# Kernel tuning notes

Measured on AMD Instinct MI355X. Metric: run time of the kernel, lower is better.

The kernel has to match this reference:

```python
import jax, jax.numpy as jnp
import numpy as np

N_NODES = 100000
N_EDGES = 1600000
N_GRAPHS = 512
EPS = 1e-12


def _glorot(key, shape):
    lim = float(np.sqrt(6.0 / (shape[0] + shape[1])))
    return jax.random.uniform(key, shape, jnp.float32, -lim, lim)


def setup_inputs() -> dict:
    key = jax.random.key(0)
    ks = jax.random.split(key, 16)
    x = jax.random.normal(ks[0], (N_NODES, 5), jnp.float32)
    edge_index = jax.random.randint(ks[1], (2, N_EDGES), 0, N_NODES)
    batch = jnp.sort(jax.random.randint(ks[2], (N_NODES,), 0, N_GRAPHS))
    return {
        "x": x,
        "edge_index": edge_index,
        "batch": batch,
        "num_graphs": N_GRAPHS,
        # pre: Linear(5, 32)
        "pre_w": _glorot(ks[3], (5, 32)), "pre_b": jnp.zeros((32,), jnp.float32),
        # conv1: SAGEConv(32, 64): lin_l (agg, bias), lin_r (root, no bias)
        "c1_wl": _glorot(ks[4], (32, 64)), "c1_bl": jnp.zeros((64,), jnp.float32),
        "c1_wr": _glorot(ks[5], (32, 64)),
        # conv2: SAGEConv(64, 64)
        "c2_wl": _glorot(ks[6], (64, 64)), "c2_bl": jnp.zeros((64,), jnp.float32),
        "c2_wr": _glorot(ks[7], (64, 64)),
        # post / out linears
        "p1_w": _glorot(ks[8], (64, 64)), "p1_b": jnp.zeros((64,), jnp.float32),
        "p2_w": _glorot(ks[9], (64, 16)), "p2_b": jnp.zeros((16,), jnp.float32),
        "o_w": _glorot(ks[10], (16, 1)), "o_b": jnp.zeros((1,), jnp.float32),
    }


def _sage_conv(x, src, dst, w_l, b_l, w_r, n_nodes):
    # mean-aggregate neighbor messages src -> dst
    msg = x[src]                                              # [E, d]
    agg = jax.ops.segment_sum(msg, dst, num_segments=n_nodes)  # [N, d]
    cnt = jax.ops.segment_sum(jnp.ones((src.shape[0], 1), x.dtype), dst,
                              num_segments=n_nodes)            # [N, 1]
    agg = jnp.where(cnt > 0, agg / jnp.maximum(cnt, 1.0), 0.0)
    out = agg @ w_l + b_l + x @ w_r
    # normalize=True -> L2 normalize per node
    nrm = jnp.linalg.norm(out, axis=-1, keepdims=True)
    return out / jnp.maximum(nrm, EPS)


def reference(x, edge_index, batch, num_graphs,
              pre_w, pre_b, c1_wl, c1_bl, c1_wr, c2_wl, c2_bl, c2_wr,
              p1_w, p1_b, p2_w, p2_b, o_w, o_b):
    n_nodes = x.shape[0]
    src, dst = edge_index[0], edge_index[1]
    h = jax.nn.relu(x @ pre_w + pre_b)
    h = jax.nn.relu(_sage_conv(h, src, dst, c1_wl, c1_bl, c1_wr, n_nodes))
    h = jax.nn.relu(_sage_conv(h, src, dst, c2_wl, c2_bl, c2_wr, n_nodes))
    # global mean pool over batch index
    s = jax.ops.segment_sum(h, batch, num_segments=num_graphs)          # [G, d]
    c = jax.ops.segment_sum(jnp.ones((n_nodes, 1), h.dtype), batch,
                            num_segments=num_graphs)                    # [G, 1]
    g = s / jnp.maximum(c, 1.0)
    g = jax.nn.relu(g @ p1_w + p1_b)
    g = jax.nn.relu(g @ p2_w + p2_b)
    out = g @ o_w + o_b
    return out.squeeze(-1)
```

## Files before the change

### kernel.cpp

```cpp
#include <hip/hip_runtime.h>

#define EPSN 1e-12f
#define TILE 2048
#define BSH 8
#define BNODES 256
#define SBMAX 512
#define BCAP 4608
#define CSRCAP 512

using frag_ab = __attribute__((ext_vector_type(8))) short;
using frag_cd = __attribute__((ext_vector_type(4))) float;
using f32x2   = __attribute__((ext_vector_type(2))) float;

template <bool B> struct BoolC { static constexpr bool value = B; };

__device__ inline unsigned short f2bf(float x) {
    union { float f; unsigned u; } v; v.f = x;
    unsigned r = v.u + 0x7fffu + ((v.u >> 16) & 1u);
    return (unsigned short)(r >> 16);
}
__device__ inline unsigned short pk2fp8(float a, float b) {
    return (unsigned short)(__builtin_amdgcn_cvt_pk_fp8_f32(a, b, 0, false) & 0xffff);
}
__device__ inline unsigned char to_fp8(float a) {
    return (unsigned char)(__builtin_amdgcn_cvt_pk_fp8_f32(a, a, 0, false) & 0xff);
}
__device__ inline void up8add(unsigned u, float* a) {
    f32x2 lo = __builtin_amdgcn_cvt_pk_f32_fp8(u, false);
    f32x2 hi = __builtin_amdgcn_cvt_pk_f32_fp8(u, true);
    a[0] += lo.x; a[1] += lo.y; a[2] += hi.x; a[3] += hi.y;
}

__global__ __launch_bounds__(256) void prep_all(
    const float* __restrict__ x, const float* __restrict__ pw,
    const float* __restrict__ pb, unsigned char* __restrict__ h0, int n,
    const float* __restrict__ w1l, const float* __restrict__ w1r,
    unsigned short* __restrict__ wpk1,
    const float* __restrict__ w2l, const float* __restrict__ w2r,
    unsigned short* __restrict__ wpk2,
    float* __restrict__ sg, int gtot,
    int* __restrict__ bcnt, int nsb) {
    int idx = blockIdx.x * 256 + threadIdx.x;
    int npre = n * 16;
    if (idx < npre) {
        int node = idx >> 4, j2 = idx & 15;
        int j = j2 * 2;
        float v0 = pb[j], v1 = pb[j + 1];
#pragma unroll
        for (int k = 0; k < 5; ++k) {
            float xv = x[node * 5 + k];
            v0 += xv * pw[k * 32 + j];
            v1 += xv * pw[k * 32 + j + 1];
        }
        ((unsigned short*)h0)[node * 16 + j2] =
            pk2fp8(fmaxf(v0, 0.f), fmaxf(v1, 0.f));
        return;
    }
    int o = idx - npre;
    if (o < 64 * 64) {
        int j = o / 64, k = o % 64;
        float v = (k < 32) ? w1l[k * 64 + j] : w1r[(k - 32) * 64 + j];
        wpk1[o] = f2bf(v);
        return;
    }
    o -= 64 * 64;
    if (o < 64 * 128) {
        int j = o / 128, k = o % 128;
        float v = (k < 64) ? w2l[k * 64 + j] : w2r[(k - 64) * 64 + j];
        wpk2[o] = f2bf(v);
        return;
    }
    o -= 64 * 128;
    if (o < gtot) { sg[o] = 0.f; return; }
    o -= gtot;
    if (o < nsb) bcnt[o] = 0;
}

__global__ __launch_bounds__(256) void scat1_k(const int* __restrict__ src,
                                               const int* __restrict__ dst,
                                               int* __restrict__ bcnt,
                                               int* __restrict__ staged, int e,
                                               int nsb) {
    __shared__ int lh[SBMAX];
    __shared__ int cur[SBMAX];
    int tid = threadIdx.x;
    for (int i = tid; i < nsb; i += 256) lh[i] = 0;
    __syncthreads();
    int base = blockIdx.x * TILE;
    int lim = min(base + TILE, e);
    for (int i = base + tid; i < lim; i += 256) atomicAdd(&lh[dst[i] >> BSH], 1);
    __syncthreads();
    for (int i = tid; i < nsb; i += 256) {
        int c = lh[i];
        int b = 0;
        if (c) b = atomicAdd(&bcnt[i], c);
        cur[i] = i * BCAP + b;
    }
    __syncthreads();
    for (int i = base + tid; i < lim; i += 256) {
        int d = dst[i];
        int p = atomicAdd(&cur[d >> BSH], 1);
        staged[p] = (src[i] << BSH) | (d & (BNODES - 1));
    }
}

__global__ __launch_bounds__(256) void scat2_k(const int* __restrict__ btot,
                                               const int* __restrict__ staged,
                                               int* __restrict__ csr,
                                               int* __restrict__ rofs,
                                               int* __restrict__ deg,
                                               int n, int nsb) {
    __shared__ int h[BNODES];
    __shared__ int cur[BNODES];
    __shared__ int wsum[8];
    int b = blockIdx.x;
    int tid = threadIdx.x;
    int lane = tid & 63, w = tid >> 6;
    int nlo = b << BSH;
    int nn = n - nlo; if (nn > BNODES) nn = BNODES;
    int lo = b * BCAP, hi = lo + btot[b];
    h[tid] = 0;
    __syncthreads();
    for (int i = lo + tid; i < hi; i += 256) atomicAdd(&h[staged[i] & (BNODES - 1)], 1);
    __syncthreads();
    int x = h[tid];
    int inc = x;
#pragma unroll
    for (int o = 1; o < 64; o <<= 1) {
        int t = __shfl_up(inc, o);
        if (lane >= o) inc += t;
    }
    if (lane == 63) wsum[w] = inc;
    __syncthreads();
    if (tid == 0) {
        int s = 0;
#pragma unroll
        for (int k = 0; k < 4; ++k) { int t = wsum[k]; wsum[k] = s; s += t; }
    }
    __syncthreads();
    int excl = inc - x + wsum[w];
    cur[tid] = excl;
    if (tid < nn) {
        rofs[nlo + tid] = lo + excl;
        deg[nlo + tid] = x;
    }
    __syncthreads();
    for (int i = lo + tid; i < hi; i += 256) {
        int v = staged[i];
        int p = atomicAdd(&cur[v & (BNODES - 1)], 1);
        csr[lo + p] = v >> BSH;
    }
}

template <int KE, bool POOL>
__global__ __launch_bounds__(256) void conv_mfma(
    const int* __restrict__ rofs, const int* __restrict__ deg,
    const int* __restrict__ csr,
    const unsigned char* __restrict__ hin, const unsigned short* __restrict__ wpk,
    const float* __restrict__ bl, const int* __restrict__ batch,
    float* __restrict__ sg, unsigned char* __restrict__ hout, int n) {
    constexpr int KT = 2 * KE;
    constexpr int ST = KT + 8;
    constexpr int KS = KT / 32;
    constexpr int LPE = KE / 4;
    constexpr int EPW = 64 / LPE;
    constexpr int RB = 16 / EPW;
    constexpr bool G4 = (LPE == 16);
    __shared__ unsigned short __attribute__((aligned(16))) Ab[16 * ST];
    __shared__ float __attribute__((aligned(16))) Nb[4][16];
    __shared__ int ro[16];
    __shared__ int dg[16];
    __shared__ int sb[16];
    __shared__ int csrL[CSRCAP];

    int tid = threadIdx.x;
    int w = tid >> 6;
    int lane = tid & 63;
    int quad = lane >> 4;
    int l16 = lane & 15;
    int base = blockIdx.x * 16;
    int ncol = w * 16 + l16;

    if (tid < 16) {
        int nd = base + tid;
        bool v = nd < n;
        ro[tid] = v ? rofs[nd] : 0;
        dg[tid] = v ? deg[nd] : 0;
        if (POOL) sb[tid] = v ? batch[nd] : -1;
    }

    frag_ab bfrag[KS];
#pragma unroll
    for (int s = 0; s < KS; ++s)
        bfrag[s] = *(const frag_ab*)&wpk[(((ncol * KS) + s) * 4 + quad) * 8];
    float bias = bl[ncol];
    __syncthreads();

    int ro0 = ro[0];
    int lastv = min(15, n - 1 - base);
    int span = ro[lastv] + dg[lastv] - ro0;
    int spanL = min(span, CSRCAP);
    for (int i = tid; i < spanL; i += 256) csrL[i] = csr[ro0 + i];

    int grp = lane / LPE;
    int p = lane % LPE;
    int beg[4], cnt[4];
#pragma unroll
    for (int i = 0; i < 4; ++i) {
        int li = w * 4 + i;
        beg[i] = ro[li] - ro0;
        cnt[i] = dg[li];
    }

    int sn = G4 ? grp : (grp & 3);
    bool doSelf = G4 || (grp >= 4);
    bool doAgg = G4 || (grp < 4);
    int snode = base + w * 4 + sn;
    unsigned selfv = 0u;
    if (doSelf && snode < n)
        selfv = *(const unsigned*)&hin[(size_t)snode * KE + p * 4];
    __syncthreads();

    float A[4][4] = {{0.f, 0.f, 0.f, 0.f}, {0.f, 0.f, 0.f, 0.f},
                     {0.f, 0.f, 0.f, 0.f}, {0.f, 0.f, 0.f, 0.f}};

    auto run_sweeps = [&](auto uselc) {
        constexpr bool USEL = decltype(uselc)::value;
        for (int s = 0;; ++s) {
            int e0 = s * 16;
            unsigned u[4][RB];
            bool act[4];
#pragma unroll
            for (int i = 0; i < 4; ++i) {
                act[i] = e0 < cnt[i];
                if (act[i]) {
#pragma unroll
                    for (int r = 0; r < RB; ++r) {
                        int ee = e0 + r * EPW + grp;
                        int cl = (ee < cnt[i]) ? ee : (cnt[i] - 1);
                        int off = beg[i] + cl;
                        int idx;
                        if (USEL || off < CSRCAP) idx = csrL[off];
                        else idx = csr[ro0 + off];
                        u[i][r] = *(const unsigned*)&hin[(size_t)idx * KE + p * 4];
                    }
                }
            }
#pragma unroll
            for (int i = 0; i < 4; ++i) {
                if (act[i]) {
#pragma unroll
                    for (int r = 0; r < RB; ++r)
                        if (e0 + r * EPW + grp < cnt[i]) up8add(u[i][r], A[i]);
                }
            }
            bool more = false;
#pragma unroll
            for (int i = 0; i < 4; ++i) more |= (e0 + 16) < cnt[i];
            if (!more) break;
        }
    };
    if (span <= CSRCAP) run_sweeps(BoolC<true>{});
    else run_sweeps(BoolC<false>{});

#pragma unroll
    for (int i = 0; i < 4; ++i) {
#pragma unroll
        for (int o = LPE; o < 64; o <<= 1) {
#pragma unroll
            for (int q = 0; q < 4; ++q) A[i][q] += __shfl_xor(A[i][q], o);
        }
    }

    float av0 = A[0][0], av1 = A[0][1], av2 = A[0][2], av3 = A[0][3];
    int cs = cnt[0];
#pragma unroll
    for (int i = 1; i < 4; ++i) {
        bool m = (sn == i);
        av0 = m ? A[i][0] : av0; av1 = m ? A[i][1] : av1;
        av2 = m ? A[i][2] : av2; av3 = m ? A[i][3] : av3;
        cs = m ? cnt[i] : cs;
    }
    {
        int li = w * 4 + sn;
        int node = base + li;
        if (node < n) {
            if (doAgg) {
                float inv = (cs > 0) ? 1.0f / (float)cs : 0.0f;
                uint2 o2;
                o2.x = (unsigned)f2bf(av0 * inv) | ((unsigned)f2bf(av1 * inv) << 16);
                o2.y = (unsigned)f2bf(av2 * inv) | ((unsigned)f2bf(av3 * inv) << 16);
                *(uint2*)&Ab[li * ST + p * 4] = o2;
            }
            if (doSelf) {
                f32x2 lo = __builtin_amdgcn_cvt_pk_f32_fp8(selfv, false);
                f32x2 hi = __builtin_amdgcn_cvt_pk_f32_fp8(selfv, true);
                uint2 o2;
                o2.x = (unsigned)f2bf(lo.x) | ((unsigned)f2bf(lo.y) << 16);
                o2.y = (unsigned)f2bf(hi.x) | ((unsigned)f2bf(hi.y) << 16);
                *(uint2*)&Ab[li * ST + KE + p * 4] = o2;
            }
        }
    }
    __syncthreads();

    frag_cd acc = (frag_cd){0.f, 0.f, 0.f, 0.f};
#pragma unroll
    for (int s = 0; s < KS; ++s) {
        frag_ab af = *(frag_ab*)&Ab[l16 * ST + s * 32 + quad * 8];
        acc = __builtin_amdgcn_mfma_f32_16x16x32_bf16(af, bfrag[s], acc, 0, 0, 0);
    }

    float vv[4], q[4];
#pragma unroll
    for (int i = 0; i < 4; ++i) {
        float v = acc[i] + bias;
        vv[i] = v;
        q[i] = v * v;
    }
#pragma unroll
    for (int o = 1; o < 16; o <<= 1) {
#pragma unroll
        for (int i = 0; i < 4; ++i) q[i] += __shfl_xor(q[i], o);
    }
    if (l16 == 0)
        *(float4*)&Nb[w][quad * 4] = make_float4(q[0], q[1], q[2], q[3]);
    __syncthreads();

    float s0 = 0.f, s1 = 0.f, s2 = 0.f, s3 = 0.f;
#pragma unroll
    for (int ww = 0; ww < 4; ++ww) {
        float4 xq = *(const float4*)&Nb[ww][quad * 4];
        s0 += xq.x; s1 += xq.y; s2 += xq.z; s3 += xq.w;
    }
    float ss[4] = {s0, s1, s2, s3};
    float pv[4];
#pragma unroll
    for (int i = 0; i < 4; ++i) {
        float nv = fmaxf(sqrtf(ss[i]), EPSN);
        pv[i] = fmaxf(vv[i] / nv, 0.f);
    }

    if (!POOL) {
#pragma unroll
        for (int i = 0; i < 4; ++i) {
            int node = base + quad * 4 + i;
            if (node < n)
                hout[(size_t)node * 64 + ncol] = to_fp8(pv[i]);
        }
    } else {
        int g0 = sb[0];
        int g1 = sb[min(15, n - 1 - base)];
        for (int g = g0; g <= g1; ++g) {
            float s = 0.f;
#pragma unroll
            for (int i = 0; i < 4; ++i)
                if (sb[quad * 4 + i] == g) s += pv[i];
            s += __shfl_xor(s, 16);
            s += __shfl_xor(s, 32);
            if (quad == 0) atomicAdd(&sg[(size_t)g * 64 + ncol], s);
        }
    }
}

__global__ __launch_bounds__(64) void mlp_k(
    const float* __restrict__ sg, const int* __restrict__ batch, int n,
    const float* __restrict__ p1w, const float* __restrict__ p1b,
    const float* __restrict__ p2w, const float* __restrict__ p2b,
    const float* __restrict__ ow, const float* __restrict__ ob,
    float* __restrict__ out) {
    __shared__ float gmean[64];
    __shared__ float a1[64];
    __shared__ float a2[16];
    int g = blockIdx.x;
    int j = threadIdx.x;
    int lo = 0, hi = n;
    while (lo < hi) { int m = (lo + hi) >> 1; if (batch[m] < g) lo = m + 1; else hi = m; }
    int start = lo;
    hi = n;
    while (lo < hi) { int m = (lo + hi) >> 1; if (batch[m] < g + 1) lo = m + 1; else hi = m; }
    float c = (float)(lo - start);
    gmean[j] = sg[(size_t)g * 64 + j] / fmaxf(c, 1.0f);
    __syncthreads();
    float v = p1b[j];
#pragma unroll 8
    for (int k = 0; k < 64; ++k) v = fmaf(gmean[k], p1w[k * 64 + j], v);
    a1[j] = fmaxf(v, 0.f);
    __syncthreads();
    if (j < 16) {
        float v2 = p2b[j];
#pragma unroll 8
        for (int k = 0; k < 64; ++k) v2 = fmaf(a1[k], p2w[k * 16 + j], v2);
        a2[j] = fmaxf(v2, 0.f);
    }
    __syncthreads();
    if (j == 0) {
        float v3 = ob[0];
#pragma unroll
        for (int k = 0; k < 16; ++k) v3 = fmaf(a2[k], ow[k], v3);
        out[g] = v3;
    }
}

extern "C" void kernel_launch(void* const* d_in, const int* in_sizes, int n_in,
                              void* d_out, int out_size, void* d_ws, size_t ws_size,
                              hipStream_t stream) {
    const float* x     = (const float*)d_in[0];
    const int*   ei    = (const int*)d_in[1];
    const int*   batch = (const int*)d_in[2];
    const float* pre_w = (const float*)d_in[4];
    const float* pre_b = (const float*)d_in[5];
    const float* c1_wl = (const float*)d_in[6];
    const float* c1_bl = (const float*)d_in[7];
    const float* c1_wr = (const float*)d_in[8];
    const float* c2_wl = (const float*)d_in[9];
    const float* c2_bl = (const float*)d_in[10];
    const float* c2_wr = (const float*)d_in[11];
    const float* p1w   = (const float*)d_in[12];
    const float* p1b   = (const float*)d_in[13];
    const float* p2w   = (const float*)d_in[14];
    const float* p2b   = (const float*)d_in[15];
    const float* ow    = (const float*)d_in[16];
    const float* ob    = (const float*)d_in[17];

    const int N = in_sizes[0] / 5;
    const int E = in_sizes[1] / 2;
    const int G = out_size;
    const int NT = (E + TILE - 1) / TILE;
    const int NSB = (N + BNODES - 1) / BNODES;
    const int* src = ei;
    const int* dst = ei + E;

    size_t h0_bytes = (((size_t)N * 32) + 127) & ~(size_t)127;
    size_t h1_bytes = (((size_t)N * 64) + 127) & ~(size_t)127;
    unsigned char* h0u = (unsigned char*)d_ws;
    unsigned char* h1u = h0u + h0_bytes;
    unsigned short* wpk1 = (unsigned short*)(h1u + h1_bytes);
    unsigned short* wpk2 = wpk1 + 64 * 64;
    float* sg    = (float*)(wpk2 + 64 * 128);
    int* rofs    = (int*)(sg + (size_t)G * 64);
    int* deg     = rofs + N;
    int* bcnt    = deg + N;
    int* staged  = bcnt + NSB;
    int* csr     = staged + (size_t)NSB * BCAP;

    int prep_tot = N * 16 + 64 * 64 + 64 * 128 + G * 64 + NSB;
    int prep_blocks = (prep_tot + 255) / 256;
    prep_all<<<prep_blocks, 256, 0, stream>>>(
        x, pre_w, pre_b, h0u, N, c1_wl, c1_wr, wpk1, c2_wl, c2_wr, wpk2,
        sg, G * 64, bcnt, NSB);

    scat1_k<<<NT, 256, 0, stream>>>(src, dst, bcnt, staged, E, NSB);
    scat2_k<<<NSB, 256, 0, stream>>>(bcnt, staged, csr, rofs, deg, N, NSB);

    conv_mfma<32, false><<<(N + 15) / 16, 256, 0, stream>>>(
        rofs, deg, csr, h0u, wpk1, c1_bl, batch, sg, h1u, N);
    conv_mfma<64, true><<<(N + 15) / 16, 256, 0, stream>>>(
        rofs, deg, csr, h1u, wpk2, c2_bl, batch, sg, nullptr, N);

    mlp_k<<<G, 64, 0, stream>>>(sg, batch, N, p1w, p1b, p2w, p2b, ow, ob,
                                (float*)d_out);
}
```

Before: 241.8 us.

## Fuse edge bucketing scatter with node/weight prep kernel and enlarge edge tile

Merges the first edge-bucketing pass into the prep kernel as extra blocks, so the scatter and the node pre-linear/weight packing run in one launch and can overlap. Zeroing of bucket counters and pooled sums moves to a small separate kernel that runs first. The edge tile grows from 2048 to 16384 edges per block, which cuts global atomics on the bucket counters but leaves only about 98 scatter blocks, each doing much more serial work. That risks poor GPU occupancy for the scatter phase.

```diff
diff --git a/kernel.cpp b/kernel.cpp
--- a/kernel.cpp
+++ b/kernel.cpp
@@ -1,7 +1,7 @@
 #include <hip/hip_runtime.h>
 
 #define EPSN 1e-12f
-#define TILE 2048
+#define TILE 16384
 #define BSH 8
 #define BNODES 256
 #define SBMAX 512
@@ -31,16 +31,48 @@
     a[0] += lo.x; a[1] += lo.y; a[2] += hi.x; a[3] += hi.y;
 }
 
-__global__ __launch_bounds__(256) void prep_all(
+__global__ __launch_bounds__(256) void zero_k(int* __restrict__ bcnt, int nsb,
+                                              float* __restrict__ sg, int gtot) {
+    int i = blockIdx.x * 256 + threadIdx.x;
+    if (i < nsb) bcnt[i] = 0;
+    else if (i < nsb + gtot) sg[i - nsb] = 0.f;
+}
+
+__global__ __launch_bounds__(256) void scat_prep(
     const float* __restrict__ x, const float* __restrict__ pw,
     const float* __restrict__ pb, unsigned char* __restrict__ h0, int n,
     const float* __restrict__ w1l, const float* __restrict__ w1r,
     unsigned short* __restrict__ wpk1,
     const float* __restrict__ w2l, const float* __restrict__ w2r,
     unsigned short* __restrict__ wpk2,
-    float* __restrict__ sg, int gtot,
-    int* __restrict__ bcnt, int nsb) {
-    int idx = blockIdx.x * 256 + threadIdx.x;
+    const int* __restrict__ src, const int* __restrict__ dst,
+    int* __restrict__ bcnt, int* __restrict__ staged, int e,
+    int nsb, int nsc) {
+    __shared__ int lh[SBMAX];
+    __shared__ int cur[SBMAX];
+    int tid = threadIdx.x;
+    if (blockIdx.x < nsc) {
+        int b0 = blockIdx.x * TILE;
+        int lim = min(b0 + TILE, e);
+        for (int i = tid; i < nsb; i += 256) lh[i] = 0;
+        __syncthreads();
+        for (int i = b0 + tid; i < lim; i += 256) atomicAdd(&lh[dst[i] >> BSH], 1);
+        __syncthreads();
+        for (int i = tid; i < nsb; i += 256) {
+            int c = lh[i];
+            int b = 0;
+            if (c) b = atomicAdd(&bcnt[i], c);
+            cur[i] = i * BCAP + b;
+        }
+        __syncthreads();
+        for (int i = b0 + tid; i < lim; i += 256) {
+            int d = dst[i];
+            int p = atomicAdd(&cur[d >> BSH], 1);
+            staged[p] = (src[i] << BSH) | (d & (BNODES - 1));
+        }
+        return;
+    }
+    int idx = (blockIdx.x - nsc) * 256 + tid;
     int npre = n * 16;
     if (idx < npre) {
         int node = idx >> 4, j2 = idx & 15;
@@ -68,39 +100,6 @@
         int j = o / 128, k = o % 128;
         float v = (k < 64) ? w2l[k * 64 + j] : w2r[(k - 64) * 64 + j];
         wpk2[o] = f2bf(v);
-        return;
-    }
-    o -= 64 * 128;
-    if (o < gtot) { sg[o] = 0.f; return; }
-    o -= gtot;
-    if (o < nsb) bcnt[o] = 0;
-}
-
-__global__ __launch_bounds__(256) void scat1_k(const int* __restrict__ src,
-                                               const int* __restrict__ dst,
-                                               int* __restrict__ bcnt,
-                                               int* __restrict__ staged, int e,
-                                               int nsb) {
-    __shared__ int lh[SBMAX];
-    __shared__ int cur[SBMAX];
-    int tid = threadIdx.x;
-    for (int i = tid; i < nsb; i += 256) lh[i] = 0;
-    __syncthreads();
-    int base = blockIdx.x * TILE;
-    int lim = min(base + TILE, e);
-    for (int i = base + tid; i < lim; i += 256) atomicAdd(&lh[dst[i] >> BSH], 1);
-    __syncthreads();
-    for (int i = tid; i < nsb; i += 256) {
-        int c = lh[i];
-        int b = 0;
-        if (c) b = atomicAdd(&bcnt[i], c);
-        cur[i] = i * BCAP + b;
-    }
-    __syncthreads();
-    for (int i = base + tid; i < lim; i += 256) {
-        int d = dst[i];
-        int p = atomicAdd(&cur[d >> BSH], 1);
-        staged[p] = (src[i] << BSH) | (d & (BNODES - 1));
     }
 }
 
@@ -426,7 +425,7 @@
     const int N = in_sizes[0] / 5;
     const int E = in_sizes[1] / 2;
     const int G = out_size;
-    const int NT = (E + TILE - 1) / TILE;
+    const int NSC = (E + TILE - 1) / TILE;
     const int NSB = (N + BNODES - 1) / BNODES;
     const int* src = ei;
     const int* dst = ei + E;
@@ -444,13 +443,15 @@
     int* staged  = bcnt + NSB;
     int* csr     = staged + (size_t)NSB * BCAP;
 
-    int prep_tot = N * 16 + 64 * 64 + 64 * 128 + G * 64 + NSB;
+    int zt = NSB + G * 64;
+    zero_k<<<(zt + 255) / 256, 256, 0, stream>>>(bcnt, NSB, sg, G * 64);
+
+    int prep_tot = N * 16 + 64 * 64 + 64 * 128;
     int prep_blocks = (prep_tot + 255) / 256;
-    prep_all<<<prep_blocks, 256, 0, stream>>>(
+    scat_prep<<<NSC + prep_blocks, 256, 0, stream>>>(
         x, pre_w, pre_b, h0u, N, c1_wl, c1_wr, wpk1, c2_wl, c2_wr, wpk2,
-        sg, G * 64, bcnt, NSB);
-
-    scat1_k<<<NT, 256, 0, stream>>>(src, dst, bcnt, staged, E, NSB);
+        src, dst, bcnt, staged, E, NSB, NSC);
+
     scat2_k<<<NSB, 256, 0, stream>>>(bcnt, staged, csr, rofs, deg, N, NSB);
 
     conv_mfma<32, false><<<(N + 15) / 16, 256, 0, stream>>>(
```

Result: slower. 256.4 us (+6.0%).
